# Optimization experiments

Hardware: AMD Instinct MI355X
Metric: run time of the kernel (lower is better)

The kernel has to match this reference:

```python
import jax, jax.numpy as jnp
import numpy as np

HIDDEN = [256, 128, 64, 32]
N_IN, N_OUT = 784, 10
V_REST = 0.0; V_RESET = 0.0; V_TH = 1.0; R_MEM = 1.0; DT = 1.0; TAU = 2.0
ALPHA = DT / TAU
SLOPE = 5.0
B, T = 128, 500


def setup_inputs() -> dict:
    key = jax.random.key(0)
    ks = jax.random.split(key, 7)
    sizes = [N_IN] + HIDDEN + [N_OUT]
    inp = {"input_spikes": jax.random.uniform(ks[0], (B, N_IN, T), dtype=jnp.float32)}
    for i in range(len(sizes) - 1):  # 5 weight matrices
        inp[f"w{i}"] = jax.random.uniform(ks[i + 1], (sizes[i], sizes[i + 1]), dtype=jnp.float32) * 0.1
    return inp


def _lif(v, cur):
    # voltage update, surrogate spike, hard reset (reset uses detached spike)
    v = v + (-(v - V_REST) + R_MEM * cur) * ALPHA
    s = jax.nn.sigmoid(SLOPE * (v - V_TH))
    sd = jax.lax.stop_gradient(s)
    v = v * (1.0 - sd) + V_RESET * sd
    return v, s


def reference(input_spikes, w0, w1, w2, w3, w4):
    ws = [jax.nn.relu(w) for w in (w0, w1, w2, w3, w4)]
    n_h = len(HIDDEN)
    b = input_spikes.shape[0]
    dt = input_spikes.dtype
    xs = jnp.transpose(input_spikes, (2, 0, 1))  # (T, B, N_IN)

    v0 = tuple(jnp.full((b, h), V_REST, dtype=dt) for h in HIDDEN)
    v_out0 = jnp.full((b, N_OUT), V_REST, dtype=dt)
    s_prev0 = tuple(jnp.zeros((b, h), dtype=dt) for h in HIDDEN)

    def step(carry, x_t):
        vs, v_out, s_prev = carry
        new_vs, new_s = [], []
        # layer 0 driven by current-step input
        v, s = _lif(vs[0], x_t @ ws[0])
        new_vs.append(v); new_s.append(s)
        # deeper hidden layers driven by PREVIOUS-step spikes (s_prev)
        for li in range(1, n_h):
            v, s = _lif(vs[li], s_prev[li - 1] @ ws[li])
            new_vs.append(v); new_s.append(s)
        # output layer driven by previous-step spikes of last hidden layer
        v_out, s_out = _lif(v_out, s_prev[-1] @ ws[-1])
        return (tuple(new_vs), v_out, tuple(new_s)), (tuple(new_s), s_out)

    _, (hs, outs) = jax.lax.scan(step, (v0, v_out0, s_prev0), xs)
    hidden_spikes = tuple(jnp.transpose(h, (1, 2, 0)) for h in hs)  # each (B, H, T)
    output_spikes = jnp.transpose(outs, (1, 2, 0))                   # (B, N_OUT, T)
    firing_rates = output_spikes.mean(axis=2)                         # (B, N_OUT)
    return (*hidden_spikes, output_spikes, firing_rates)
```

## Files before the change

### kernel.cpp

```cpp
#include <hip/hip_runtime.h>

#define NIN 784
#define H0 256
#define H1 128
#define H2 64
#define H3 32
#define NOUT 10
#define BATCH 128
#define TT 500
#define KCH0 25
#define JTILES 16

#define SW1 136
#define SW2 72
#define SW3 40
#define CW1 132
#define CW2 68
#define CW3 36
#define CW4 20
#define OW4 12

#define H1_OFF (BATCH * H0 * TT)
#define H2_OFF (H1_OFF + BATCH * H1 * TT)
#define H3_OFF (H2_OFF + BATCH * H2 * TT)
#define OUT_OFF (H3_OFF + BATCH * H3 * TT)
#define RATE_OFF (OUT_OFF + BATCH * NOUT * TT)

typedef __attribute__((ext_vector_type(8))) short short8v;
typedef __attribute__((ext_vector_type(4))) float f32x4;

__device__ __forceinline__ unsigned short f2bf(float f) {
  union { float f; unsigned u; } v; v.f = f;
  unsigned r = v.u + 0x7FFFu + ((v.u >> 16) & 1u);
  return (unsigned short)(r >> 16);
}
__device__ __forceinline__ float bf2f(unsigned short b) {
  union { unsigned u; float f; } v; v.u = ((unsigned)b) << 16;
  return v.f;
}

__device__ __forceinline__ float lif_step(float& v, float c) {
  v = 0.5f * (v + c);
  const float E = __expf(5.0f * (1.0f - v));
  const float r = 1.0f / (1.0f + E);
  v = v * E * r;
  return r;
}

__global__ void pack_all(const float* __restrict__ w0, const float* __restrict__ w1,
                         const float* __restrict__ w2, const float* __restrict__ w3,
                         const float* __restrict__ w4, unsigned short* __restrict__ Wf,
                         unsigned short* __restrict__ Bf) {
  const int bid = blockIdx.x, l = threadIdx.x;
  if (bid < JTILES * KCH0) {
    const int jt = bid / KCH0, kc = bid % KCH0;
    const int j = jt * 16 + (l & 15);
    const int kbase = kc * 32 + (l >> 4) * 8;
    unsigned v[4];
#pragma unroll
    for (int e = 0; e < 4; ++e) {
      const int k0 = kbase + e * 2;
      const float f0 = (k0 < NIN) ? fmaxf(w0[(size_t)k0 * H0 + j], 0.0f) : 0.0f;
      const float f1 = (k0 + 1 < NIN) ? fmaxf(w0[(size_t)(k0 + 1) * H0 + j], 0.0f) : 0.0f;
      v[e] = (unsigned)f2bf(f0) | ((unsigned)f2bf(f1) << 16);
    }
    uint4 o; o.x = v[0]; o.y = v[1]; o.z = v[2]; o.w = v[3];
    reinterpret_cast<uint4*>(Wf)[(size_t)bid * 64 + l] = o;
    return;
  }
  const int tile = bid - JTILES * KCH0;
  const float* w; int K, Nw, base, rel, KCH;
  if (tile < 64)      { w = w1; K = 256; Nw = 128; base = 0;        rel = tile;      KCH = 8; }
  else if (tile < 80) { w = w2; K = 128; Nw = 64;  base = 64 * 512; rel = tile - 64; KCH = 4; }
  else if (tile < 84) { w = w3; K = 64;  Nw = 32;  base = 80 * 512; rel = tile - 80; KCH = 2; }
  else                { w = w4; K = 32;  Nw = 10;  base = 84 * 512; rel = 0;         KCH = 1; }
  const int nt = rel / KCH, kc = rel % KCH;
  const int n = nt * 16 + (l & 15);
  const int kb = kc * 32 + (l >> 4) * 8;
  unsigned v[4];
#pragma unroll
  for (int e = 0; e < 4; ++e) {
    const int k0 = kb + e * 2;
    const float f0 = (n < Nw && k0 < K)     ? fmaxf(w[(size_t)k0 * Nw + n], 0.0f) : 0.0f;
    const float f1 = (n < Nw && k0 + 1 < K) ? fmaxf(w[(size_t)(k0 + 1) * Nw + n], 0.0f) : 0.0f;
    v[e] = (unsigned)f2bf(f0) | ((unsigned)f2bf(f1) << 16);
  }
  uint4 o; o.x = v[0]; o.y = v[1]; o.z = v[2]; o.w = v[3];
  *reinterpret_cast<uint4*>(Bf + base + ((size_t)rel * 64 + l) * 8) = o;
}

__global__ __launch_bounds__(256, 4) void gemm0(
    const float* __restrict__ X, const unsigned short* __restrict__ Wf,
    unsigned short* __restrict__ cur0) {
  const int ttile = blockIdx.x;
  const int b = blockIdx.y;
  const int tid = threadIdx.x;
  const int wave = tid >> 6, lane = tid & 63;
  const int t0 = ttile * 64;
  __shared__ unsigned short Xs[2][64 * 40];
  f32x4 acc[4][4];
#pragma unroll
  for (int i = 0; i < 4; ++i)
#pragma unroll
    for (int jj = 0; jj < 4; ++jj) acc[i][jj] = (f32x4)0.0f;

  const float* Xb = X + (size_t)b * NIN * TT;
  const int tt = tid & 63;
  const int kb = wave * 2;
  const int lrow = lane & 15, lgrp = lane >> 4;
  const int tgl = t0 + tt;
  const bool tin = tgl < TT;

  float r[8];
#pragma unroll
  for (int pp = 0; pp < 4; ++pp) {
    const int k = kb + pp * 8;
    r[pp * 2]     = tin ? Xb[(size_t)k * TT + tgl] : 0.0f;
    r[pp * 2 + 1] = tin ? Xb[(size_t)(k + 1) * TT + tgl] : 0.0f;
  }

  for (int kc = 0; kc < KCH0; ++kc) {
    unsigned short* xbuf = Xs[kc & 1];
#pragma unroll
    for (int pp = 0; pp < 4; ++pp) {
      const unsigned pk = (unsigned)f2bf(r[pp * 2]) | ((unsigned)f2bf(r[pp * 2 + 1]) << 16);
      *reinterpret_cast<unsigned*>(&xbuf[tt * 40 + kb + pp * 8]) = pk;
    }
    __syncthreads();
    if (kc + 1 < KCH0) {
      const int k0 = (kc + 1) * 32;
#pragma unroll
      for (int pp = 0; pp < 4; ++pp) {
        const int k = k0 + kb + pp * 8;
        r[pp * 2]     = (tin && k < NIN)     ? Xb[(size_t)k * TT + tgl] : 0.0f;
        r[pp * 2 + 1] = (tin && k + 1 < NIN) ? Xb[(size_t)(k + 1) * TT + tgl] : 0.0f;
      }
    }
    short8v afr[4], bfr[4];
#pragma unroll
    for (int jf = 0; jf < 4; ++jf) {
      const size_t off = ((size_t)((wave * 4 + jf) * KCH0 + kc) * 64 + lane) * 8;
      afr[jf] = *reinterpret_cast<const short8v*>(Wf + off);
    }
#pragma unroll
    for (int tf = 0; tf < 4; ++tf)
      bfr[tf] = *reinterpret_cast<const short8v*>(&xbuf[(tf * 16 + lrow) * 40 + lgrp * 8]);
#pragma unroll
    for (int jf = 0; jf < 4; ++jf)
#pragma unroll
      for (int tf = 0; tf < 4; ++tf)
        acc[jf][tf] = __builtin_amdgcn_mfma_f32_16x16x32_bf16(afr[jf], bfr[tf], acc[jf][tf], 0, 0, 0);
    __syncthreads();
  }

#pragma unroll
  for (int tf = 0; tf < 4; ++tf) {
    const int t = t0 + tf * 16 + lrow;
    if (t >= TT) continue;
    unsigned short* row = cur0 + ((size_t)b * TT + t) * H0;
#pragma unroll
    for (int jf = 0; jf < 4; ++jf) {
      const int j = wave * 64 + jf * 16 + lgrp * 4;
      const f32x4 a = acc[jf][tf];
      const unsigned p0 = (unsigned)f2bf(a[0]) | ((unsigned)f2bf(a[1]) << 16);
      const unsigned p1 = (unsigned)f2bf(a[2]) | ((unsigned)f2bf(a[3]) << 16);
      *reinterpret_cast<unsigned*>(row + j) = p0;
      *reinterpret_cast<unsigned*>(row + j + 2) = p1;
    }
  }
}

__global__ __launch_bounds__(64) void scan0(
    const unsigned short* __restrict__ cur0, unsigned short* __restrict__ s0g,
    float* __restrict__ out) {
  const int b = blockIdx.y, jg = blockIdx.x, l = threadIdx.x;
  const int j = jg * 64 + l;
  const unsigned short* cp = cur0 + (size_t)b * TT * H0 + j;
  unsigned short* sp = s0g + (size_t)b * 512 * H0 + j;
  float* hp = out + ((size_t)b * H0 + j) * TT;
  sp[0] = 0;
  float v = 0.0f;
  float c0[16], c1[16];
#define LOAD16(D, T0) _Pragma("unroll") for (int u = 0; u < 16; ++u) (D)[u] = bf2f(cp[(size_t)((T0) + u) * H0]);
#define PROC16(C, T0)                                                                \
  do {                                                                               \
    float hb[16];                                                                    \
    _Pragma("unroll")                                                                \
    for (int u = 0; u < 16; ++u) {                                                   \
      const float s = lif_step(v, (C)[u]);                                           \
      hb[u] = s;                                                                     \
      sp[(size_t)((T0) + u + 1) * H0] = f2bf(s);                                     \
    }                                                                                \
    _Pragma("unroll")                                                                \
    for (int q = 0; q < 4; ++q)                                                      \
      *reinterpret_cast<float4*>(hp + (T0) + q * 4) =                                \
          make_float4(hb[q * 4], hb[q * 4 + 1], hb[q * 4 + 2], hb[q * 4 + 3]);       \
  } while (0)
  LOAD16(c0, 0);
  for (int i = 0; i < 15; ++i) {
    const int tb = i * 32;
    LOAD16(c1, tb + 16);
    PROC16(c0, tb);
    LOAD16(c0, tb + 32);
    PROC16(c1, tb + 16);
  }
  PROC16(c0, 480);
  {
    float c[4], hb[4];
#pragma unroll
    for (int u = 0; u < 4; ++u) c[u] = bf2f(cp[(size_t)(496 + u) * H0]);
#pragma unroll
    for (int u = 0; u < 4; ++u) {
      const float s = lif_step(v, c[u]);
      hb[u] = s;
      sp[(size_t)(496 + u + 1) * H0] = f2bf(s);
    }
    *reinterpret_cast<float4*>(hp + 496) = make_float4(hb[0], hb[1], hb[2], hb[3]);
  }
#undef LOAD16
#undef PROC16
}

template<int N>
__device__ __forceinline__ void lif_lds(float& v, float& rate, const unsigned short* cur,
                                        int cw, unsigned short* sd, int sw) {
  float cr[16];
  const unsigned short* cp = cur;
#pragma unroll
  for (int u = 0; u < N; ++u) { cr[u] = bf2f(*cp); cp += cw; }
#pragma unroll
  for (int u = 0; u < N; ++u) {
    const float s = lif_step(v, cr[u]);
    *sd = f2bf(s); sd += sw;
    rate += s;
  }
}

__global__ __launch_bounds__(512, 1) void snn_tail14(
    const unsigned short* __restrict__ s0g, const unsigned short* __restrict__ Bf,
    float* __restrict__ out) {
  __shared__ __align__(16) unsigned short wl[85 * 512];
  __shared__ __align__(16) unsigned short s1b[65 * SW1];
  __shared__ __align__(16) unsigned short s2b[65 * SW2];
  __shared__ __align__(16) unsigned short s3b[65 * SW3];
  __shared__ __align__(16) unsigned short c1b[64 * CW1];
  __shared__ __align__(16) unsigned short c2b[64 * CW2];
  __shared__ __align__(16) unsigned short c3b[64 * CW3];
  __shared__ __align__(16) unsigned short c4b[64 * CW4];
  __shared__ __align__(16) unsigned short o4b[64 * OW4];

  const int b = blockIdx.x, tid = threadIdx.x;
  const int w = tid >> 6, lane = tid & 63, lr = lane & 15, lg = lane >> 4;
  const unsigned short* WL1 = wl;
  const unsigned short* WL2 = wl + 64 * 512;
  const unsigned short* WL3 = wl + 80 * 512;
  const unsigned short* WL4 = wl + 84 * 512;
  const unsigned short* s0b = s0g + (size_t)b * 512 * H0;

  {
    const uint4* src = reinterpret_cast<const uint4*>(Bf);
    uint4* dst = reinterpret_cast<uint4*>(wl);
    for (int i = tid; i < 85 * 512 / 8; i += 512) dst[i] = src[i];
  }

  float v = 0.0f, rate = 0.0f;
  int lay = 0, j = 0;
  const unsigned short* curb = nullptr;
  unsigned short* sb = s3b;
  int cw = 0, sw = 0;
  bool srow0 = false, sact = false;
  unsigned short* sdbase = nullptr;
  if (tid < 128) {
    lay = 1; j = tid; curb = c1b + j; sb = s1b; cw = CW1; sw = SW1;
    srow0 = true; sact = true; sdbase = s1b + j + SW1;
  } else if (tid < 192) {
    lay = 2; j = tid - 128; curb = c2b + j; sb = s2b; cw = CW2; sw = SW2;
    srow0 = true; sact = true; sdbase = s2b + j + SW2;
  } else if (tid < 224) {
    lay = 3; j = tid - 192; curb = c3b + j; sb = s3b; cw = CW3; sw = SW3;
    srow0 = true; sact = true; sdbase = s3b + j + SW3;
  } else if (tid < 240) {
    lay = 4; j = tid - 224; curb = c4b + j; cw = CW4; sw = OW4;
    srow0 = false; sact = (j < NOUT); sdbase = o4b + j;
  }
  __syncthreads();

  for (int p = 0; p < 12; ++p) {
    short8v a1[8];
    if (p <= 7) {
      const int tt = w >> 1;
      const unsigned short* ap = s0b + (size_t)(p * 64 + tt * 16 + lr) * H0 + lg * 8;
#pragma unroll
      for (int kc = 0; kc < 8; ++kc) a1[kc] = *reinterpret_cast<const short8v*>(ap + kc * 32);
    }
    if (sact) {
      const int c = p - lay;
      if (c >= 0 && c <= 7) {
        if (srow0) sb[j] = (c == 0) ? (unsigned short)0 : sb[64 * sw + j];
        if (c < 7) {
#pragma unroll
          for (int q = 0; q < 4; ++q)
            lif_lds<16>(v, rate, curb + q * 16 * cw, cw, sdbase + q * 16 * sw, sw);
        } else {
          lif_lds<16>(v, rate, curb, cw, sdbase, sw);
          lif_lds<16>(v, rate, curb + 16 * cw, cw, sdbase + 16 * sw, sw);
          lif_lds<16>(v, rate, curb + 32 * cw, cw, sdbase + 32 * sw, sw);
          lif_lds<4>(v, rate, curb + 48 * cw, cw, sdbase + 48 * sw, sw);
        }
      }
    }
    __syncthreads();
    if (p <= 7) {
      const int tt = w >> 1, nb = (w & 1) * 4;
#pragma unroll
      for (int n4 = 0; n4 < 4; ++n4) {
        const int nt = nb + n4;
        f32x4 acc = (f32x4)0.0f;
#pragma unroll
        for (int kc = 0; kc < 8; ++kc) {
          const short8v bf = *reinterpret_cast<const short8v*>(WL1 + ((size_t)(nt * 8 + kc) * 64 + lane) * 8);
          acc = __builtin_amdgcn_mfma_f32_16x16x32_bf16(a1[kc], bf, acc, 0, 0, 0);
        }
        unsigned short* cd = c1b + (tt * 16 + lg * 4) * CW1 + nt * 16 + lr;
#pragma unroll
        for (int r = 0; r < 4; ++r) cd[r * CW1] = f2bf(acc[r]);
      }
    }
    if (p >= 1 && p <= 8) {
      const int tt = w >> 1;
      short8v a[4];
      const unsigned short* ap = s1b + (tt * 16 + lr) * SW1 + lg * 8;
#pragma unroll
      for (int kc = 0; kc < 4; ++kc) a[kc] = *reinterpret_cast<const short8v*>(ap + kc * 32);
#pragma unroll
      for (int qi = 0; qi < 2; ++qi) {
        const int nt = (w & 1) * 2 + qi;
        f32x4 acc = (f32x4)0.0f;
#pragma unroll
        for (int kc = 0; kc < 4; ++kc) {
          const short8v bf = *reinterpret_cast<const short8v*>(WL2 + ((size_t)(nt * 4 + kc) * 64 + lane) * 8);
          acc = __builtin_amdgcn_mfma_f32_16x16x32_bf16(a[kc], bf, acc, 0, 0, 0);
        }
        unsigned short* cd = c2b + (tt * 16 + lg * 4) * CW2 + nt * 16 + lr;
#pragma unroll
        for (int r = 0; r < 4; ++r) cd[r * CW2] = f2bf(acc[r]);
      }
    }
    if (p >= 2 && p <= 9) {
      const int tt = w >> 1, nt = w & 1;
      short8v a[2];
      const unsigned short* ap = s2b + (tt * 16 + lr) * SW2 + lg * 8;
#pragma unroll
      for (int kc = 0; kc < 2; ++kc) a[kc] = *reinterpret_cast<const short8v*>(ap + kc * 32);
      f32x4 acc = (f32x4)0.0f;
#pragma unroll
      for (int kc = 0; kc < 2; ++kc) {
        const short8v bf = *reinterpret_cast<const short8v*>(WL3 + ((size_t)(nt * 2 + kc) * 64 + lane) * 8);
        acc = __builtin_amdgcn_mfma_f32_16x16x32_bf16(a[kc], bf, acc, 0, 0, 0);
      }
      unsigned short* cd = c3b + (tt * 16 + lg * 4) * CW3 + nt * 16 + lr;
#pragma unroll
      for (int r = 0; r < 4; ++r) cd[r * CW3] = f2bf(acc[r]);
    }
    if (p >= 3 && p <= 10 && w < 4) {
      const int tt = w;
      const unsigned short* ap = s3b + (tt * 16 + lr) * SW3 + lg * 8;
      const short8v a0 = *reinterpret_cast<const short8v*>(ap);
      const short8v bf = *reinterpret_cast<const short8v*>(WL4 + (size_t)lane * 8);
      f32x4 acc = (f32x4)0.0f;
      acc = __builtin_amdgcn_mfma_f32_16x16x32_bf16(a0, bf, acc, 0, 0, 0);
      unsigned short* cd = c4b + (tt * 16 + lg * 4) * CW4 + lr;
#pragma unroll
      for (int r = 0; r < 4; ++r) cd[r * CW4] = f2bf(acc[r]);
    }
    if (p >= 1 && p <= 8) {
      const int c = p - 1;
      const int nt = (c == 7) ? 52 : 64;
      if (lane < nt) {
        float* o1 = out + H1_OFF + ((size_t)b * H1 + w * 16) * TT + c * 64 + lane;
#pragma unroll
        for (int rr = 0; rr < 16; ++rr)
          o1[(size_t)rr * TT] = bf2f(s1b[(lane + 1) * SW1 + w * 16 + rr]);
      }
    }
    if (p >= 2 && p <= 9) {
      const int c = p - 2;
      const int nt = (c == 7) ? 52 : 64;
      if (lane < nt) {
        float* o2 = out + H2_OFF + ((size_t)b * H2 + w * 8) * TT + c * 64 + lane;
#pragma unroll
        for (int rr = 0; rr < 8; ++rr)
          o2[(size_t)rr * TT] = bf2f(s2b[(lane + 1) * SW2 + w * 8 + rr]);
      }
    }
    if (p >= 3 && p <= 10) {
      const int c = p - 3;
      const int nt = (c == 7) ? 52 : 64;
      if (lane < nt) {
        float* o3 = out + H3_OFF + ((size_t)b * H3 + w * 4) * TT + c * 64 + lane;
#pragma unroll
        for (int rr = 0; rr < 4; ++rr)
          o3[(size_t)rr * TT] = bf2f(s3b[(lane + 1) * SW3 + w * 4 + rr]);
      }
    }
    if (p >= 4 && p <= 11 && w < 5) {
      const int c = p - 4;
      const int nt = (c == 7) ? 52 : 64;
      if (lane < nt) {
#pragma unroll
        for (int rr = 0; rr < 2; ++rr) {
          const int jj = w * 2 + rr;
          out[OUT_OFF + ((size_t)b * NOUT + jj) * TT + c * 64 + lane] =
              bf2f(o4b[lane * OW4 + jj]);
        }
      }
    }
    __syncthreads();
  }
  if (tid >= 224 && tid < 224 + NOUT)
    out[RATE_OFF + (size_t)b * NOUT + (tid - 224)] = rate * (1.0f / (float)TT);
}

extern "C" void kernel_launch(void* const* d_in, const int* in_sizes, int n_in,
                              void* d_out, int out_size, void* d_ws, size_t ws_size,
                              hipStream_t stream) {
  const float* X  = (const float*)d_in[0];
  const float* w0 = (const float*)d_in[1];
  const float* w1 = (const float*)d_in[2];
  const float* w2 = (const float*)d_in[3];
  const float* w3 = (const float*)d_in[4];
  const float* w4 = (const float*)d_in[5];
  float* out = (float*)d_out;

  uint8_t* ws = (uint8_t*)d_ws;
  const size_t SLOT = 33554432;
  unsigned short* cur0 = (unsigned short*)ws;
  unsigned short* s0g  = (unsigned short*)(ws + SLOT);
  unsigned short* Wf0  = (unsigned short*)(ws + 2 * SLOT);
  unsigned short* Bf2  = Wf0 + (size_t)JTILES * KCH0 * 64 * 8;

  pack_all<<<JTILES * KCH0 + 85, 64, 0, stream>>>(w0, w1, w2, w3, w4, Wf0, Bf2);
  gemm0<<<dim3(8, BATCH), 256, 0, stream>>>(X, Wf0, cur0);
  scan0<<<dim3(4, BATCH), 64, 0, stream>>>(cur0, s0g, out);
  snn_tail14<<<BATCH, 512, 0, stream>>>(s0g, Bf2, out);
}
```

Before: 190.1 us.

## Hoist layer-1 GEMM into separate kernel and unroll gemm0 K-loop by two

Layer-1 current computation moves out of the serial tail kernel into a new fully parallel GEMM kernel that writes bf16 currents to global memory, reusing the cur0 workspace slot. The tail kernel now only copies 64-timestep tiles of precomputed currents into a double-buffered LDS slot, which shortens its per-phase critical path and shrinks its weight LDS footprint. gemm0's K loop is manually unrolled by two with ping-pong register prefetch buffers. This adds an extra kernel launch plus a global round trip for the layer-1 currents.

```diff
diff --git a/kernel.cpp b/kernel.cpp
--- a/kernel.cpp
+++ b/kernel.cpp
@@ -14,7 +14,6 @@
 #define SW1 136
 #define SW2 72
 #define SW3 40
-#define CW1 132
 #define CW2 68
 #define CW3 36
 #define CW4 20
@@ -111,47 +110,49 @@
   const int tgl = t0 + tt;
   const bool tin = tgl < TT;
 
-  float r[8];
-#pragma unroll
-  for (int pp = 0; pp < 4; ++pp) {
-    const int k = kb + pp * 8;
-    r[pp * 2]     = tin ? Xb[(size_t)k * TT + tgl] : 0.0f;
-    r[pp * 2 + 1] = tin ? Xb[(size_t)(k + 1) * TT + tgl] : 0.0f;
-  }
-
-  for (int kc = 0; kc < KCH0; ++kc) {
-    unsigned short* xbuf = Xs[kc & 1];
-#pragma unroll
-    for (int pp = 0; pp < 4; ++pp) {
-      const unsigned pk = (unsigned)f2bf(r[pp * 2]) | ((unsigned)f2bf(r[pp * 2 + 1]) << 16);
-      *reinterpret_cast<unsigned*>(&xbuf[tt * 40 + kb + pp * 8]) = pk;
-    }
-    __syncthreads();
-    if (kc + 1 < KCH0) {
-      const int k0 = (kc + 1) * 32;
-#pragma unroll
-      for (int pp = 0; pp < 4; ++pp) {
-        const int k = k0 + kb + pp * 8;
-        r[pp * 2]     = (tin && k < NIN)     ? Xb[(size_t)k * TT + tgl] : 0.0f;
-        r[pp * 2 + 1] = (tin && k + 1 < NIN) ? Xb[(size_t)(k + 1) * TT + tgl] : 0.0f;
-      }
-    }
-    short8v afr[4], bfr[4];
-#pragma unroll
-    for (int jf = 0; jf < 4; ++jf) {
-      const size_t off = ((size_t)((wave * 4 + jf) * KCH0 + kc) * 64 + lane) * 8;
-      afr[jf] = *reinterpret_cast<const short8v*>(Wf + off);
-    }
-#pragma unroll
-    for (int tf = 0; tf < 4; ++tf)
-      bfr[tf] = *reinterpret_cast<const short8v*>(&xbuf[(tf * 16 + lrow) * 40 + lgrp * 8]);
-#pragma unroll
-    for (int jf = 0; jf < 4; ++jf)
-#pragma unroll
-      for (int tf = 0; tf < 4; ++tf)
-        acc[jf][tf] = __builtin_amdgcn_mfma_f32_16x16x32_bf16(afr[jf], bfr[tf], acc[jf][tf], 0, 0, 0);
-    __syncthreads();
-  }
+#define LOADX(R, KC)                                                            \
+  do {                                                                          \
+    const int k0_ = (KC) * 32;                                                  \
+    _Pragma("unroll") for (int pp = 0; pp < 4; ++pp) {                          \
+      const int k_ = k0_ + kb + pp * 8;                                         \
+      (R)[pp * 2]     = (tin && k_ < NIN)     ? Xb[(size_t)k_ * TT + tgl] : 0.0f; \
+      (R)[pp * 2 + 1] = (tin && k_ + 1 < NIN) ? Xb[(size_t)(k_ + 1) * TT + tgl] : 0.0f; \
+    }                                                                           \
+  } while (0)
+
+#define GBODY(R, KC, PFKC)                                                      \
+  do {                                                                          \
+    unsigned short* xbuf = Xs[(KC) & 1];                                        \
+    _Pragma("unroll") for (int pp = 0; pp < 4; ++pp) {                          \
+      const unsigned pk = (unsigned)f2bf((R)[pp * 2]) |                         \
+                          ((unsigned)f2bf((R)[pp * 2 + 1]) << 16);              \
+      *reinterpret_cast<unsigned*>(&xbuf[tt * 40 + kb + pp * 8]) = pk;          \
+    }                                                                           \
+    __syncthreads();                                                            \
+    if ((PFKC) < KCH0) LOADX(R, PFKC);                                          \
+    short8v afr[4], bfr[4];                                                     \
+    _Pragma("unroll") for (int jf = 0; jf < 4; ++jf) {                          \
+      const size_t off = ((size_t)((wave * 4 + jf) * KCH0 + (KC)) * 64 + lane) * 8; \
+      afr[jf] = *reinterpret_cast<const short8v*>(Wf + off);                    \
+    }                                                                           \
+    _Pragma("unroll") for (int tf = 0; tf < 4; ++tf)                            \
+      bfr[tf] = *reinterpret_cast<const short8v*>(&xbuf[(tf * 16 + lrow) * 40 + lgrp * 8]); \
+    _Pragma("unroll") for (int jf = 0; jf < 4; ++jf)                            \
+      _Pragma("unroll") for (int tf = 0; tf < 4; ++tf)                          \
+        acc[jf][tf] = __builtin_amdgcn_mfma_f32_16x16x32_bf16(afr[jf], bfr[tf], acc[jf][tf], 0, 0, 0); \
+    __syncthreads();                                                            \
+  } while (0)
+
+  float rA[8], rB[8];
+  LOADX(rA, 0);
+  LOADX(rB, 1);
+  for (int i = 0; i < 12; ++i) {
+    GBODY(rA, 2 * i, 2 * i + 2);
+    GBODY(rB, 2 * i + 1, 2 * i + 3);
+  }
+  GBODY(rA, 24, 99);
+#undef LOADX
+#undef GBODY
 
 #pragma unroll
   for (int tf = 0; tf < 4; ++tf) {
@@ -221,6 +222,37 @@
 #undef PROC16
 }
 
+__global__ __launch_bounds__(256) void gemm1full(
+    const unsigned short* __restrict__ s0g, const unsigned short* __restrict__ Bf,
+    unsigned short* __restrict__ cur1g) {
+  __shared__ __align__(16) unsigned short wl1[64 * 512];
+  const int b = blockIdx.y, tid = threadIdx.x;
+  const int w = tid >> 6, lane = tid & 63, lr = lane & 15, lg = lane >> 4;
+  {
+    const uint4* src = reinterpret_cast<const uint4*>(Bf);
+    uint4* dst = reinterpret_cast<uint4*>(wl1);
+    for (int i = tid; i < 64 * 512 / 8; i += 256) dst[i] = src[i];
+  }
+  const int t0 = blockIdx.x * 64 + w * 16;
+  const unsigned short* ap = s0g + ((size_t)b * 512 + t0 + lr) * H0 + lg * 8;
+  short8v a[8];
+#pragma unroll
+  for (int kc = 0; kc < 8; ++kc) a[kc] = *reinterpret_cast<const short8v*>(ap + kc * 32);
+  __syncthreads();
+  unsigned short* cb = cur1g + ((size_t)b * 512 + t0 + lg * 4) * H1 + lr;
+#pragma unroll
+  for (int nt = 0; nt < 8; ++nt) {
+    f32x4 acc = (f32x4)0.0f;
+#pragma unroll
+    for (int kc = 0; kc < 8; ++kc) {
+      const short8v bf = *reinterpret_cast<const short8v*>(wl1 + ((size_t)(nt * 8 + kc) * 64 + lane) * 8);
+      acc = __builtin_amdgcn_mfma_f32_16x16x32_bf16(a[kc], bf, acc, 0, 0, 0);
+    }
+#pragma unroll
+    for (int r = 0; r < 4; ++r) cb[(size_t)r * H1 + nt * 16] = f2bf(acc[r]);
+  }
+}
+
 template<int N>
 __device__ __forceinline__ void lif_lds(float& v, float& rate, const unsigned short* cur,
                                         int cw, unsigned short* sd, int sw) {
@@ -236,14 +268,14 @@
   }
 }
 
-__global__ __launch_bounds__(512, 1) void snn_tail14(
-    const unsigned short* __restrict__ s0g, const unsigned short* __restrict__ Bf,
+__global__ __launch_bounds__(512, 1) void snn_tail(
+    const unsigned short* __restrict__ cur1g, const unsigned short* __restrict__ Bf,
     float* __restrict__ out) {
-  __shared__ __align__(16) unsigned short wl[85 * 512];
+  __shared__ __align__(16) unsigned short wl[21 * 512];
   __shared__ __align__(16) unsigned short s1b[65 * SW1];
   __shared__ __align__(16) unsigned short s2b[65 * SW2];
   __shared__ __align__(16) unsigned short s3b[65 * SW3];
-  __shared__ __align__(16) unsigned short c1b[64 * CW1];
+  __shared__ __align__(16) unsigned short c1b[2][64 * H1];
   __shared__ __align__(16) unsigned short c2b[64 * CW2];
   __shared__ __align__(16) unsigned short c3b[64 * CW3];
   __shared__ __align__(16) unsigned short c4b[64 * CW4];
@@ -251,16 +283,15 @@
 
   const int b = blockIdx.x, tid = threadIdx.x;
   const int w = tid >> 6, lane = tid & 63, lr = lane & 15, lg = lane >> 4;
-  const unsigned short* WL1 = wl;
-  const unsigned short* WL2 = wl + 64 * 512;
-  const unsigned short* WL3 = wl + 80 * 512;
-  const unsigned short* WL4 = wl + 84 * 512;
-  const unsigned short* s0b = s0g + (size_t)b * 512 * H0;
+  const unsigned short* WL2 = wl;
+  const unsigned short* WL3 = wl + 16 * 512;
+  const unsigned short* WL4 = wl + 20 * 512;
+  const unsigned short* cur1b = cur1g + (size_t)b * 512 * H1;
 
   {
-    const uint4* src = reinterpret_cast<const uint4*>(Bf);
+    const uint4* src = reinterpret_cast<const uint4*>(Bf + 64 * 512);
     uint4* dst = reinterpret_cast<uint4*>(wl);
-    for (int i = tid; i < 85 * 512 / 8; i += 512) dst[i] = src[i];
+    for (int i = tid; i < 21 * 512 / 8; i += 512) dst[i] = src[i];
   }
 
   float v = 0.0f, rate = 0.0f;
@@ -271,7 +302,7 @@
   bool srow0 = false, sact = false;
   unsigned short* sdbase = nullptr;
   if (tid < 128) {
-    lay = 1; j = tid; curb = c1b + j; sb = s1b; cw = CW1; sw = SW1;
+    lay = 1; j = tid; sb = s1b; cw = H1; sw = SW1;
     srow0 = true; sact = true; sdbase = s1b + j + SW1;
   } else if (tid < 192) {
     lay = 2; j = tid - 128; curb = c2b + j; sb = s2b; cw = CW2; sw = SW2;
@@ -286,45 +317,29 @@
   __syncthreads();
 
   for (int p = 0; p < 12; ++p) {
-    short8v a1[8];
-    if (p <= 7) {
-      const int tt = w >> 1;
-      const unsigned short* ap = s0b + (size_t)(p * 64 + tt * 16 + lr) * H0 + lg * 8;
-#pragma unroll
-      for (int kc = 0; kc < 8; ++kc) a1[kc] = *reinterpret_cast<const short8v*>(ap + kc * 32);
-    }
     if (sact) {
       const int c = p - lay;
       if (c >= 0 && c <= 7) {
+        const unsigned short* curp = (lay == 1) ? (&c1b[(p - 1) & 1][0] + j) : curb;
         if (srow0) sb[j] = (c == 0) ? (unsigned short)0 : sb[64 * sw + j];
         if (c < 7) {
 #pragma unroll
           for (int q = 0; q < 4; ++q)
-            lif_lds<16>(v, rate, curb + q * 16 * cw, cw, sdbase + q * 16 * sw, sw);
+            lif_lds<16>(v, rate, curp + q * 16 * cw, cw, sdbase + q * 16 * sw, sw);
         } else {
-          lif_lds<16>(v, rate, curb, cw, sdbase, sw);
-          lif_lds<16>(v, rate, curb + 16 * cw, cw, sdbase + 16 * sw, sw);
-          lif_lds<16>(v, rate, curb + 32 * cw, cw, sdbase + 32 * sw, sw);
-          lif_lds<4>(v, rate, curb + 48 * cw, cw, sdbase + 48 * sw, sw);
+          lif_lds<16>(v, rate, curp, cw, sdbase, sw);
+          lif_lds<16>(v, rate, curp + 16 * cw, cw, sdbase + 16 * sw, sw);
+          lif_lds<16>(v, rate, curp + 32 * cw, cw, sdbase + 32 * sw, sw);
+          lif_lds<4>(v, rate, curp + 48 * cw, cw, sdbase + 48 * sw, sw);
         }
       }
     }
     __syncthreads();
     if (p <= 7) {
-      const int tt = w >> 1, nb = (w & 1) * 4;
-#pragma unroll
-      for (int n4 = 0; n4 < 4; ++n4) {
-        const int nt = nb + n4;
-        f32x4 acc = (f32x4)0.0f;
-#pragma unroll
-        for (int kc = 0; kc < 8; ++kc) {
-          const short8v bf = *reinterpret_cast<const short8v*>(WL1 + ((size_t)(nt * 8 + kc) * 64 + lane) * 8);
-          acc = __builtin_amdgcn_mfma_f32_16x16x32_bf16(a1[kc], bf, acc, 0, 0, 0);
-        }
-        unsigned short* cd = c1b + (tt * 16 + lg * 4) * CW1 + nt * 16 + lr;
-#pragma unroll
-        for (int r = 0; r < 4; ++r) cd[r * CW1] = f2bf(acc[r]);
-      }
+      const uint4* src = reinterpret_cast<const uint4*>(cur1b + (size_t)p * 64 * H1);
+      uint4* dst = reinterpret_cast<uint4*>(&c1b[p & 1][0]);
+      dst[tid] = src[tid];
+      dst[tid + 512] = src[tid + 512];
     }
     if (p >= 1 && p <= 8) {
       const int tt = w >> 1;
@@ -434,13 +449,15 @@
 
   uint8_t* ws = (uint8_t*)d_ws;
   const size_t SLOT = 33554432;
-  unsigned short* cur0 = (unsigned short*)ws;
-  unsigned short* s0g  = (unsigned short*)(ws + SLOT);
-  unsigned short* Wf0  = (unsigned short*)(ws + 2 * SLOT);
-  unsigned short* Bf2  = Wf0 + (size_t)JTILES * KCH0 * 64 * 8;
+  unsigned short* cur0  = (unsigned short*)ws;
+  unsigned short* cur1g = (unsigned short*)ws;
+  unsigned short* s0g   = (unsigned short*)(ws + SLOT);
+  unsigned short* Wf0   = (unsigned short*)(ws + 2 * SLOT);
+  unsigned short* Bf2   = Wf0 + (size_t)JTILES * KCH0 * 64 * 8;
 
   pack_all<<<JTILES * KCH0 + 85, 64, 0, stream>>>(w0, w1, w2, w3, w4, Wf0, Bf2);
   gemm0<<<dim3(8, BATCH), 256, 0, stream>>>(X, Wf0, cur0);
   scan0<<<dim3(4, BATCH), 64, 0, stream>>>(cur0, s0g, out);
-  snn_tail14<<<BATCH, 512, 0, stream>>>(s0g, Bf2, out);
-}
+  gemm1full<<<dim3(8, BATCH), 256, 0, stream>>>(s0g, Bf2, cur1g);
+  snn_tail<<<BATCH, 512, 0, stream>>>(cur1g, Bf2, out);
+}
```

Result: slower. 211.4 us (+11.2%).
